# Performance work log

Measured on AMD Instinct MI355X. Metric: run time of the kernel, lower is better.

The kernel has to match this reference:

```python
import jax, jax.numpy as jnp
import numpy as np

H = 512      # hidden == embed (required: process-block LSTM consumes attention output of size hidden)
XY = 2
CITY_T = 100
BATCH = 512
INIT = 0.08  # uniform(-0.08, 0.08) weight init


def _unif(key, shape):
    return jax.random.uniform(key, shape, jnp.float32, minval=-INIT, maxval=INIT)


def lstm_cell(x, h, c, Wih, Whh, bih, bhh):
    # PyTorch gate order: i, f, g, o
    g = x @ Wih.T + h @ Whh.T + (bih + bhh)
    i, f, gg, o = jnp.split(g, 4, axis=-1)
    c_new = jax.nn.sigmoid(f) * c + jax.nn.sigmoid(i) * jnp.tanh(gg)
    h_new = jax.nn.sigmoid(o) * jnp.tanh(c_new)
    return h_new, c_new


def setup_inputs() -> dict:
    key = jax.random.key(0)
    ks = jax.random.split(key, 20)
    inp = {
        "x": jax.random.uniform(ks[0], (BATCH, CITY_T, XY), jnp.float32),      # city coords in [0,1)
        "dec_i1": jax.random.uniform(ks[1], (BATCH, H), jnp.float32),          # torch.rand(batch,1,hidden)
        "W_emb": _unif(ks[2], (H, XY)),
        "enc_Wih": _unif(ks[3], (4 * H, H)),
        "enc_Whh": _unif(ks[4], (4 * H, H)),
        "enc_bih": _unif(ks[5], (4 * H,)),
        "enc_bhh": _unif(ks[6], (4 * H,)),
        "dec_Wih": _unif(ks[7], (4 * H, H)),
        "dec_Whh": _unif(ks[8], (4 * H, H)),
        "dec_bih": _unif(ks[9], (4 * H,)),
        "dec_bhh": _unif(ks[10], (4 * H,)),
        "W_q": _unif(ks[11], (H, H)),
        "W_ref": _unif(ks[12], (H, H)),
        "v": _unif(ks[13], (1, H)),       # Vec: Linear(hidden,1,bias=False)
        "fc1": _unif(ks[14], (H, H)),
        "fc2": _unif(ks[15], (1, H)),
    }
    return inp


def reference(x, dec_i1, W_emb, enc_Wih, enc_Whh, enc_bih, enc_bhh,
              dec_Wih, dec_Whh, dec_bih, dec_bhh, W_q, W_ref, v, fc1, fc2):
    batch, city_t, _ = x.shape
    emb = x @ W_emb.T                                   # (b, c, H)

    # ---- Encoder LSTM (zero initial state) ----
    h0 = jnp.zeros((batch, H), emb.dtype)
    c0 = jnp.zeros((batch, H), emb.dtype)

    def enc_step(carry, xt):
        h, c = carry
        h, c = lstm_cell(xt, h, c, enc_Wih, enc_Whh, enc_bih, enc_bhh)
        return (h, c), h

    (hT, cT), enc_h = jax.lax.scan(enc_step, (h0, c0), jnp.swapaxes(emb, 0, 1))
    enc_h = jnp.swapaxes(enc_h, 0, 1)                   # (b, c, H)

    # W_ref(enc_h) is static across decode steps -> compute once
    u1 = enc_h @ W_ref.T                                # (b, c, H)

    # ---- Decoder: city_t steps of LSTM cell + Bahdanau attention ----
    def dec_step(carry, _):
        dec_i, h, c = carry
        h, c = lstm_cell(dec_i, h, c, dec_Wih, dec_Whh, dec_bih, dec_bhh)
        u2 = h @ W_q.T                                  # (b, H)
        u = jnp.tanh(u1 + u2[:, None, :]) @ v[0]        # (b, c)
        a = jax.nn.softmax(u, axis=1)
        d = jnp.einsum('bc,bch->bh', a, enc_h)          # glimpse (b, H)
        return (d, h, c), None

    (_, h_last, _), _ = jax.lax.scan(dec_step, (dec_i1, hT, cT), None, length=city_t)

    # final2FC: Linear->ReLU->Linear -> scalar per batch
    pred_l = jax.nn.relu(h_last @ fc1.T) @ fc2.T        # (b, 1)
    return pred_l[:, 0]
```

## Files before the change

kernel.cpp:

```cpp
#include <hip/hip_runtime.h>
#include <hip/hip_bf16.h>

#define H 512
#define TSTEPS 100
#define BATCH 512
#define KB 16
#define NBLK 256
#define NT 1024
#define NGRP 8
#define GBLK 32

typedef __attribute__((ext_vector_type(8))) short bf16x8;
typedef __attribute__((ext_vector_type(8))) unsigned short u16x8;
typedef __attribute__((ext_vector_type(4))) float f32x4;
typedef unsigned short u16;

__device__ __forceinline__ float bf2f(u16 u) {
    union { unsigned int i; float f; } z; z.i = ((unsigned int)u) << 16; return z.f;
}
__device__ __forceinline__ u16 f2bf(float f) {
    union { float f; unsigned int u; } z; z.f = f;
    unsigned int r = (z.u + 0x7fffu + ((z.u >> 16) & 1u)) >> 16;
    return (u16)r;
}
__device__ __forceinline__ float sigmoidf_(float x) { return 1.0f / (1.0f + __expf(-x)); }
__device__ __forceinline__ float ftanh(float x) {
    x = fminf(15.0f, fmaxf(-15.0f, x));
    float e = __expf(2.0f * x);
    return (e - 1.0f) / (e + 1.0f);
}
__device__ __forceinline__ f32x4 MF(bf16x8 a, bf16x8 b, f32x4 c) {
    return __builtin_amdgcn_mfma_f32_16x16x32_bf16(a, b, c, 0, 0, 0);
}

__device__ __forceinline__ size_t pidx(int m, int k) {
    int kb = k >> 5, kin = k & 31;
    int lane = (m & 15) + (((kin >> 2) & 3) << 4);
    int j = (kin & 3) + ((kin >> 4) << 2);
    return ((size_t)((m >> 4) * KB + kb) * 64 + lane) * 8 + j;
}

__device__ __forceinline__ void gbar32(unsigned* bar, int grp) {
    __syncthreads();
    if (threadIdx.x == 0) {
        unsigned* cnt = &bar[grp * 32];
        unsigned* gen = &bar[grp * 32 + 16];
        unsigned g = __hip_atomic_load(gen, __ATOMIC_RELAXED, __HIP_MEMORY_SCOPE_AGENT);
        if (__hip_atomic_fetch_add(cnt, 1u, __ATOMIC_ACQ_REL, __HIP_MEMORY_SCOPE_AGENT) == GBLK - 1u) {
            __hip_atomic_store(cnt, 0u, __ATOMIC_RELAXED, __HIP_MEMORY_SCOPE_AGENT);
            __hip_atomic_fetch_add(gen, 1u, __ATOMIC_ACQ_REL, __HIP_MEMORY_SCOPE_AGENT);
        } else {
            while (__hip_atomic_load(gen, __ATOMIC_RELAXED, __HIP_MEMORY_SCOPE_AGENT) == g) {
                __builtin_amdgcn_s_sleep(2);
            }
            __threadfence();
        }
    }
    __syncthreads();
}

__global__ void prep_kernel(const float* __restrict__ W_emb, const float* __restrict__ enc_Wih,
                            const float* __restrict__ enc_bih, const float* __restrict__ enc_bhh,
                            const float* __restrict__ dec_bih, const float* __restrict__ dec_bhh,
                            float* __restrict__ Wc, float* __restrict__ bc, float* __restrict__ db) {
    int g = blockIdx.x * blockDim.x + threadIdx.x;
    if (g >= 4 * H) return;
    float s0 = 0.f, s1 = 0.f;
    for (int j = 0; j < H; ++j) {
        float w = enc_Wih[(size_t)g * H + j];
        s0 += w * W_emb[j * 2 + 0];
        s1 += w * W_emb[j * 2 + 1];
    }
    Wc[g * 2 + 0] = s0; Wc[g * 2 + 1] = s1;
    bc[g] = enc_bih[g] + enc_bhh[g];
    db[g] = dec_bih[g] + dec_bhh[g];
}

__global__ void pack_w(const float* __restrict__ W, u16* __restrict__ hi, u16* __restrict__ lo,
                       int total) {
    int idx = blockIdx.x * 256 + threadIdx.x;
    if (idx >= total) return;
    int m = idx >> 9, k = idx & 511;
    float v = W[idx];
    u16 h16 = f2bf(v);
    u16 l16 = f2bf(v - bf2f(h16));
    size_t p = pidx(m, k);
    hi[p] = h16; lo[p] = l16;
}

__global__ void zero4(float* __restrict__ p, int n) {
    int i = blockIdx.x * blockDim.x + threadIdx.x;
    if (i < n) p[i] = 0.f;
}

__global__ __launch_bounds__(NT, 1) void persist_enc(
    const float* __restrict__ x, const float* __restrict__ Wc, const float* __restrict__ bc,
    const u16* __restrict__ WeH, const u16* __restrict__ WeL,
    float* __restrict__ cbuf, u16* __restrict__ hbuf,
    u16* __restrict__ ench, unsigned* __restrict__ bar) {
    extern __shared__ char smem[];
    u16* wlds = (u16*)smem;
    float* exch = (float*)(smem + 131072);
    const int tid = threadIdx.x;
    const int lane = tid & 63;
    const int w = tid >> 6;
    const int q = w & 3, j = w >> 2;
    const int blk = blockIdx.x;
    const int grp = blk & 7, nni = blk >> 3;
    const size_t BHs = (size_t)BATCH * H;

    for (int c = 0; c < 8; ++c) {
        int cq = c >> 1, hl = c & 1;
        const u16x8* s8 = (const u16x8*)((hl ? WeL : WeH) + (size_t)((cq * 32 + nni) * KB) * 512);
        u16x8* d8 = (u16x8*)(wlds + c * 8192);
        for (int i = tid; i < 1024; i += NT) d8[i] = s8[i];
    }
    __syncthreads();

    for (int t = 0; t < TSTEPS; ++t) {
        const u16* Ah = hbuf + (size_t)(t & 1) * 2 * BHs;
        const u16* Al = Ah + BHs;
        u16* Hh = hbuf + (size_t)((t + 1) & 1) * 2 * BHs;
        u16* Hl = Hh + BHs;
        f32x4 acc = {};
#pragma unroll 4
        for (int kb = 0; kb < KB; ++kb) {
            bf16x8 bh = *(const bf16x8*)&wlds[((q * 2 + 0) * KB + kb) * 512 + lane * 8];
            bf16x8 bl = *(const bf16x8*)&wlds[((q * 2 + 1) * KB + kb) * 512 + lane * 8];
            size_t ab = ((size_t)((grp * 4 + j) * KB + kb) * 64 + lane) * 8;
            bf16x8 ah = *(const bf16x8*)&Ah[ab];
            bf16x8 al = *(const bf16x8*)&Al[ab];
            acc = MF(ah, bh, acc);
            acc = MF(ah, bl, acc);
            acc = MF(al, bh, acc);
        }
        const int col = lane & 15, rg = lane >> 4;
#pragma unroll
        for (int r = 0; r < 4; ++r)
            exch[(q * 64 + j * 16 + rg * 4 + r) * 16 + col] = acc[r];
        __syncthreads();
        {
            int lb = tid >> 4, cl = tid & 15;
            int b = grp * 64 + lb, n = nni * 16 + cl;
            float x0 = x[((size_t)b * TSTEPS + t) * 2 + 0];
            float x1 = x[((size_t)b * TSTEPS + t) * 2 + 1];
            float g[4];
#pragma unroll
            for (int qq = 0; qq < 4; ++qq)
                g[qq] = exch[(qq * 64 + lb) * 16 + cl] + bc[qq * H + n]
                      + x0 * Wc[(qq * H + n) * 2 + 0] + x1 * Wc[(qq * H + n) * 2 + 1];
            size_t ci = (size_t)b * H + n;
            float cn = sigmoidf_(g[1]) * cbuf[ci] + sigmoidf_(g[0]) * ftanh(g[2]);
            float hn = sigmoidf_(g[3]) * ftanh(cn);
            cbuf[ci] = cn;
            u16 hh = f2bf(hn), hl16 = f2bf(hn - bf2f(hh));
            size_t p = pidx(b, n);
            Hh[p] = hh; Hl[p] = hl16;
            ench[((size_t)b * TSTEPS + t) * H + n] = hh;
        }
        gbar32(bar, grp);
    }
}

__global__ __launch_bounds__(NT, 1) void persist_dec(
    const u16* __restrict__ WdiH, const u16* __restrict__ WdiL,
    const u16* __restrict__ WdhH, const u16* __restrict__ WdhL,
    const float* __restrict__ db,
    const u16* __restrict__ WqH, const u16* __restrict__ WqL,
    const u16* __restrict__ u1r, const u16* __restrict__ ench, const float* __restrict__ vv,
    float* __restrict__ cbuf, u16* __restrict__ hbuf,
    u16* __restrict__ dhi, u16* __restrict__ dlo,
    unsigned* __restrict__ bar) {
    extern __shared__ char smem[];
    u16* wlds = (u16*)smem;
    char* scratch = smem + 131072;
    float* exch  = (float*)scratch;
    float* u2row = (float*)scratch;
    float* ssc   = (float*)(scratch + 4096);
    float* ssm   = (float*)(scratch + 4928);
    f32x4* dacc  = (f32x4*)(scratch + 5760);
    const int tid = threadIdx.x;
    const int lane = tid & 63;
    const int w = tid >> 6;
    const int blk = blockIdx.x;
    const int grp = blk & 7, nni = blk >> 3;
    const size_t BHs = (size_t)BATCH * H;

    float vvr[8];
    {
        float4 v0 = *(const float4*)&vv[lane * 8];
        float4 v1 = *(const float4*)&vv[lane * 8 + 4];
        vvr[0] = v0.x; vvr[1] = v0.y; vvr[2] = v0.z; vvr[3] = v0.w;
        vvr[4] = v1.x; vvr[5] = v1.y; vvr[6] = v1.z; vvr[7] = v1.w;
    }

    for (int c = 0; c < 8; ++c) {
        int mat = c >> 2, cq = c & 3;
        const u16x8* s8 = (const u16x8*)((mat ? WdhH : WdiH) + (size_t)((cq * 32 + nni) * KB) * 512);
        u16x8* d8 = (u16x8*)(wlds + c * 8192);
        for (int i = tid; i < 1024; i += NT) d8[i] = s8[i];
    }
    __syncthreads();

    for (int s = 0; s < TSTEPS; ++s) {
        {
            const u16* hAh = hbuf + (size_t)(s & 1) * 2 * BHs;
            const u16* hAl = hAh + BHs;
            u16* Hh = hbuf + (size_t)((s + 1) & 1) * 2 * BHs;
            u16* Hl = Hh + BHs;
            const int q = w & 3, j = w >> 2;
            f32x4 acc = {};
#pragma unroll
            for (int ph = 0; ph < 2; ++ph) {
                const u16* Ah = ph ? hAh : dhi;
                const u16* Al = ph ? hAl : dlo;
                const u16* Wl = ph ? WdhL : WdiL;
#pragma unroll 4
                for (int kb = 0; kb < KB; ++kb) {
                    bf16x8 bh = *(const bf16x8*)&wlds[((ph * 4 + q) * KB + kb) * 512 + lane * 8];
                    bf16x8 bl = *(const bf16x8*)&Wl[((size_t)((q * 32 + nni) * KB + kb) * 64 + lane) * 8];
                    size_t ab = ((size_t)((grp * 4 + j) * KB + kb) * 64 + lane) * 8;
                    bf16x8 ah = *(const bf16x8*)&Ah[ab];
                    bf16x8 al = *(const bf16x8*)&Al[ab];
                    acc = MF(ah, bh, acc);
                    acc = MF(ah, bl, acc);
                    acc = MF(al, bh, acc);
                }
            }
            const int col = lane & 15, rg = lane >> 4;
#pragma unroll
            for (int r = 0; r < 4; ++r)
                exch[(q * 64 + j * 16 + rg * 4 + r) * 16 + col] = acc[r];
            __syncthreads();
            {
                int lb = tid >> 4, cl = tid & 15;
                int b = grp * 64 + lb, n = nni * 16 + cl;
                float g[4];
#pragma unroll
                for (int qq = 0; qq < 4; ++qq)
                    g[qq] = exch[(qq * 64 + lb) * 16 + cl] + db[qq * H + n];
                size_t ci = (size_t)b * H + n;
                float cn = sigmoidf_(g[1]) * cbuf[ci] + sigmoidf_(g[0]) * ftanh(g[2]);
                float hn = sigmoidf_(g[3]) * ftanh(cn);
                cbuf[ci] = cn;
                u16 hh = f2bf(hn), hl16 = f2bf(hn - bf2f(hh));
                size_t p = pidx(b, n);
                Hh[p] = hh; Hl[p] = hl16;
            }
        }
        if (s == TSTEPS - 1) break;
        gbar32(bar, grp);

        {
            const u16* Ah = hbuf + (size_t)((s + 1) & 1) * 2 * BHs;
            const u16* Al = Ah + BHs;
            const int mf = grp * 4 + (nni >> 3);
            f32x4 acc[2] = {};
#pragma unroll 4
            for (int kb = 0; kb < KB; ++kb) {
                size_t ab = ((size_t)(mf * KB + kb) * 64 + lane) * 8;
                bf16x8 ah = *(const bf16x8*)&Ah[ab];
                bf16x8 al = *(const bf16x8*)&Al[ab];
#pragma unroll
                for (int f = 0; f < 2; ++f) {
                    int n16 = w * 2 + f;
                    size_t fb = ((size_t)(n16 * KB + kb) * 64 + lane) * 8;
                    bf16x8 bh = *(const bf16x8*)&WqH[fb];
                    bf16x8 bl = *(const bf16x8*)&WqL[fb];
                    acc[f] = MF(ah, bh, acc[f]);
                    acc[f] = MF(ah, bl, acc[f]);
                    acc[f] = MF(al, bh, acc[f]);
                }
            }
            const int col = lane & 15, rg = lane >> 4;
            const int t0 = (nni & 7) * 2;
#pragma unroll
            for (int f = 0; f < 2; ++f)
#pragma unroll
                for (int r = 0; r < 4; ++r) {
                    int m = rg * 4 + r;
                    int n = (w * 2 + f) * 16 + col;
                    if (m == t0)     u2row[n] = acc[f][r];
                    if (m == t0 + 1) u2row[512 + n] = acc[f][r];
                }
        }
        __syncthreads();
        {
            const int r = tid >> 9;
            const int par = (tid >> 6) & 7;
            const int cnt = (par < 4) ? 13 : 12;
            const int b = grp * 64 + 2 * nni + r;
            float u2v[8];
            {
                float4 a0 = *(const float4*)&u2row[r * 512 + lane * 8];
                float4 a1 = *(const float4*)&u2row[r * 512 + lane * 8 + 4];
                u2v[0] = a0.x; u2v[1] = a0.y; u2v[2] = a0.z; u2v[3] = a0.w;
                u2v[4] = a1.x; u2v[5] = a1.y; u2v[6] = a1.z; u2v[7] = a1.w;
            }
            const u16* u1base = &u1r[(size_t)b * TSTEPS * H + lane * 8];
            const u16* ehbase = &ench[(size_t)b * TSTEPS * H + lane * 8];
            for (int i0 = 0; i0 < 13; i0 += 5) {
                u16x8 uvv[5];
#pragma unroll
                for (int u = 0; u < 5; ++u) {
                    int i = i0 + u;
                    if (i < cnt)
                        uvv[u] = *(const u16x8*)&u1base[(size_t)(par + 8 * i) * H];
                }
#pragma unroll
                for (int u = 0; u < 5; ++u) {
                    int i = i0 + u;
                    if (i < cnt) {
                        float pp = 0.f;
#pragma unroll
                        for (int jj = 0; jj < 8; ++jj)
                            pp += vvr[jj] * ftanh(bf2f(uvv[u][jj]) + u2v[jj]);
#pragma unroll
                        for (int off = 32; off; off >>= 1) pp += __shfl_xor(pp, off);
                        if (lane == 0) ssc[r * 100 + par + 8 * i] = pp;
                    }
                }
            }
            __syncthreads();
            if (tid < 128) {
                int r2 = tid >> 6, ln = tid & 63;
                float s1 = ssc[r2 * 100 + ln];
                float s2 = (ln + 64 < 100) ? ssc[r2 * 100 + ln + 64] : -1e30f;
                float m = fmaxf(s1, s2);
#pragma unroll
                for (int off = 32; off; off >>= 1) m = fmaxf(m, __shfl_xor(m, off));
                float e1 = __expf(s1 - m);
                float e2 = (ln + 64 < 100) ? __expf(s2 - m) : 0.f;
                float sum = e1 + e2;
#pragma unroll
                for (int off = 32; off; off >>= 1) sum += __shfl_xor(sum, off);
                float inv = 1.f / sum;
                ssm[r2 * 100 + ln] = e1 * inv;
                if (ln + 64 < 100) ssm[r2 * 100 + ln + 64] = e2 * inv;
            }
            __syncthreads();
            float ga[8] = {};
            for (int i0 = 0; i0 < 13; i0 += 5) {
                u16x8 evv[5];
#pragma unroll
                for (int u = 0; u < 5; ++u) {
                    int i = i0 + u;
                    if (i < cnt)
                        evv[u] = *(const u16x8*)&ehbase[(size_t)(par + 8 * i) * H];
                }
#pragma unroll
                for (int u = 0; u < 5; ++u) {
                    int i = i0 + u;
                    if (i < cnt) {
                        float a = ssm[r * 100 + par + 8 * i];
#pragma unroll
                        for (int jj = 0; jj < 8; ++jj) ga[jj] += a * bf2f(evv[u][jj]);
                    }
                }
            }
            f32x4 g0 = {ga[0], ga[1], ga[2], ga[3]};
            f32x4 g1 = {ga[4], ga[5], ga[6], ga[7]};
            if (par < 4) {
                dacc[(((par * 2 + r) * 64) + lane) * 2 + 0] = g0;
                dacc[(((par * 2 + r) * 64) + lane) * 2 + 1] = g1;
            }
            __syncthreads();
            if (par >= 4) {
                int slot = par - 4;
                f32x4 t0 = dacc[(((slot * 2 + r) * 64) + lane) * 2 + 0];
                f32x4 t1 = dacc[(((slot * 2 + r) * 64) + lane) * 2 + 1];
                dacc[(((slot * 2 + r) * 64) + lane) * 2 + 0] = t0 + g0;
                dacc[(((slot * 2 + r) * 64) + lane) * 2 + 1] = t1 + g1;
            }
            __syncthreads();
            if (tid < 128) {
                int r2 = tid >> 6, l = tid & 63;
                float fin[8];
#pragma unroll
                for (int jj = 0; jj < 8; ++jj) fin[jj] = 0.f;
#pragma unroll
                for (int sl = 0; sl < 4; ++sl) {
                    f32x4 d0 = dacc[(((sl * 2 + r2) * 64) + l) * 2 + 0];
                    f32x4 d1 = dacc[(((sl * 2 + r2) * 64) + l) * 2 + 1];
                    fin[0] += d0[0]; fin[1] += d0[1]; fin[2] += d0[2]; fin[3] += d0[3];
                    fin[4] += d1[0]; fin[5] += d1[1]; fin[6] += d1[2]; fin[7] += d1[3];
                }
                int b2 = grp * 64 + 2 * nni + r2;
                int h0 = l * 8;
#pragma unroll
                for (int qd = 0; qd < 2; ++qd) {
                    int k = h0 + 4 * qd;
                    size_t p = (((size_t)(b2 >> 4) * KB + (k >> 5)) * 64 + (b2 & 15)
                                + (((k >> 2) & 3) << 4)) * 8 + (((k >> 4) & 1) << 2);
                    float f0 = fin[4 * qd], f1 = fin[4 * qd + 1], f2 = fin[4 * qd + 2], f3 = fin[4 * qd + 3];
                    u16 a0 = f2bf(f0), a1 = f2bf(f1), a2 = f2bf(f2), a3 = f2bf(f3);
                    *(ushort4*)&dhi[p] = make_ushort4(a0, a1, a2, a3);
                    u16 c0 = f2bf(f0 - bf2f(a0)), c1 = f2bf(f1 - bf2f(a1));
                    u16 c2 = f2bf(f2 - bf2f(a2)), c3 = f2bf(f3 - bf2f(a3));
                    *(ushort4*)&dlo[p] = make_ushort4(c0, c1, c2, c3);
                }
            }
        }
        gbar32(bar, grp);
    }
}

__global__ __launch_bounds__(256) void gemm_u1(const u16* __restrict__ ench_row,
                                               const u16* __restrict__ Bh, const u16* __restrict__ Bl,
                                               u16* __restrict__ u1_row) {
    __shared__ u16 lds[2 * KB * 64 * 8];
    const int tid = threadIdx.x;
    const int m0 = blockIdx.x * 32;
    {
        int r = tid >> 3;
        int o = tid & 7;
#pragma unroll
        for (int p8 = 0; p8 < 8; ++p8) {
            int k0 = (o + 8 * p8) * 8;
            const u16* src = &ench_row[(size_t)(m0 + r) * H + k0];
            ushort4 v0 = *(const ushort4*)&src[0];
            ushort4 v1 = *(const ushort4*)&src[4];
            int kb = k0 >> 5, kin0 = k0 & 31;
            int g0 = (kin0 >> 2) & 3;
            int jo = (kin0 >> 4) << 2;
            u16* base = &lds[(size_t)(((r >> 4) * KB + kb) * 64) * 8];
            *(ushort4*)&base[((r & 15) + 16 * g0) * 8 + jo] = v0;
            *(ushort4*)&base[((r & 15) + 16 * (g0 + 1)) * 8 + jo] = v1;
        }
    }
    __syncthreads();
    const int lane = tid & 63;
    const int w = tid >> 6;
    const int mw = w & 1, nh = w >> 1;
    for (int nc = 0; nc < 16; ++nc) {
        int n16 = nh * 16 + nc;
        f32x4 acc = {};
#pragma unroll 4
        for (int kb = 0; kb < KB; ++kb) {
            bf16x8 a = *(const bf16x8*)&lds[((mw * KB + kb) * 64 + lane) * 8];
            size_t fb = ((size_t)(n16 * KB + kb) * 64 + lane) * 8;
            bf16x8 bh = *(const bf16x8*)&Bh[fb];
            bf16x8 bl = *(const bf16x8*)&Bl[fb];
            acc = MF(a, bh, acc);
            acc = MF(a, bl, acc);
        }
        const int col = lane & 15, rg = lane >> 4;
#pragma unroll
        for (int r = 0; r < 4; ++r) {
            size_t mrow = (size_t)m0 + mw * 16 + rg * 4 + r;
            u1_row[mrow * H + n16 * 16 + col] = f2bf(acc[r]);
        }
    }
}

__global__ __launch_bounds__(256) void final_kernel(const u16* __restrict__ hi,
                                                    const u16* __restrict__ lo,
                                                    const float* __restrict__ fc1,
                                                    const float* __restrict__ fc2,
                                                    float* __restrict__ out) {
    const int b = blockIdx.x;
    __shared__ float hsh[H];
    __shared__ float red[256];
    for (int i = threadIdx.x; i < H; i += 256) {
        size_t p = pidx(b, i);
        hsh[i] = bf2f(hi[p]) + bf2f(lo[p]);
    }
    __syncthreads();
    float total = 0.f;
    for (int n = threadIdx.x; n < H; n += 256) {
        float acc = 0.f;
        for (int j = 0; j < H; ++j) acc += fc1[(size_t)n * H + j] * hsh[j];
        total += fmaxf(acc, 0.f) * fc2[n];
    }
    red[threadIdx.x] = total;
    __syncthreads();
    for (int s = 128; s > 0; s >>= 1) {
        if (threadIdx.x < s) red[threadIdx.x] += red[threadIdx.x + s];
        __syncthreads();
    }
    if (threadIdx.x == 0) out[b] = red[0];
}

extern "C" void kernel_launch(void* const* d_in, const int* in_sizes, int n_in,
                              void* d_out, int out_size, void* d_ws, size_t ws_size,
                              hipStream_t stream) {
    (void)in_sizes; (void)n_in; (void)out_size;
    const float* x       = (const float*)d_in[0];
    const float* dec_i1  = (const float*)d_in[1];
    const float* W_emb   = (const float*)d_in[2];
    const float* enc_Wih = (const float*)d_in[3];
    const float* enc_Whh = (const float*)d_in[4];
    const float* enc_bih = (const float*)d_in[5];
    const float* enc_bhh = (const float*)d_in[6];
    const float* dec_Wih = (const float*)d_in[7];
    const float* dec_Whh = (const float*)d_in[8];
    const float* dec_bih = (const float*)d_in[9];
    const float* dec_bhh = (const float*)d_in[10];
    const float* W_q     = (const float*)d_in[11];
    const float* W_ref   = (const float*)d_in[12];
    const float* vv      = (const float*)d_in[13];
    const float* fc1     = (const float*)d_in[14];
    const float* fc2     = (const float*)d_in[15];
    float* out = (float*)d_out;

    const size_t BH = (size_t)BATCH * H;
    const size_t W4 = (size_t)4 * H * H;
    const size_t WS = (size_t)H * H;
    const size_t TBH = (size_t)TSTEPS * BATCH * H;

    unsigned* bar = (unsigned*)d_ws;
    float* c_  = (float*)d_ws + 256;
    u16* hbuf  = (u16*)(c_ + BH);
    float* Wc  = (float*)(hbuf + 4 * BH);
    float* bc  = Wc + 4 * H * 2;
    float* db  = bc + 4 * H;
    u16* dhi   = (u16*)(db + 4 * H);
    u16* dlo   = dhi + BH;
    u16* WeH   = dlo + BH;    u16* WeL  = WeH + W4;
    u16* WdiH  = WeL + W4;    u16* WdiL = WdiH + W4;
    u16* WdhH  = WdiL + W4;   u16* WdhL = WdhH + W4;
    u16* WqH   = WdhL + W4;   u16* WqL  = WqH + WS;
    u16* WrH   = WqL + WS;    u16* WrL  = WrH + WS;
    u16* ench  = WrL + WS;
    u16* u1r   = ench + TBH;

    size_t needed = (size_t)((char*)(u1r + TBH) - (char*)d_ws);
    if (ws_size < needed) return;

    const int ENC_SMEM = 131072 + 16384;
    const int DEC_SMEM = 131072 + 22528;
    (void)hipFuncSetAttribute((const void*)persist_enc, hipFuncAttributeMaxDynamicSharedMemorySize, ENC_SMEM);
    (void)hipFuncSetAttribute((const void*)persist_dec, hipFuncAttributeMaxDynamicSharedMemorySize, DEC_SMEM);

    prep_kernel<<<8, 256, 0, stream>>>(W_emb, enc_Wih, enc_bih, enc_bhh, dec_bih, dec_bhh, Wc, bc, db);
    pack_w<<<(int)(W4 / 256), 256, 0, stream>>>(enc_Whh, WeH, WeL, (int)W4);
    pack_w<<<(int)(W4 / 256), 256, 0, stream>>>(dec_Wih, WdiH, WdiL, (int)W4);
    pack_w<<<(int)(W4 / 256), 256, 0, stream>>>(dec_Whh, WdhH, WdhL, (int)W4);
    pack_w<<<(int)(WS / 256), 256, 0, stream>>>(W_q, WqH, WqL, (int)WS);
    pack_w<<<(int)(WS / 256), 256, 0, stream>>>(W_ref, WrH, WrL, (int)WS);
    pack_w<<<(int)(BH / 256), 256, 0, stream>>>(dec_i1, dhi, dlo, (int)BH);
    zero4<<<(int)((256 + 3 * BH + 255) / 256), 256, 0, stream>>>((float*)d_ws, (int)(256 + 3 * BH));

    persist_enc<<<NBLK, NT, ENC_SMEM, stream>>>(x, Wc, bc, WeH, WeL, c_, hbuf, ench, bar);
    gemm_u1<<<TSTEPS * BATCH / 32, 256, 0, stream>>>(ench, WrH, WrL, u1r);
    persist_dec<<<NBLK, NT, DEC_SMEM, stream>>>(WdiH, WdiL, WdhH, WdhL, db, WqH, WqL,
                                                u1r, ench, vv, c_, hbuf, dhi, dlo, bar);
    final_kernel<<<BATCH, 256, 0, stream>>>(hbuf, hbuf + BH, fc1, fc2, out);
}
```

Baseline: 12.25 ms.

## Replace counter grid barrier with per-block flag barrier and prefetch glimpse rows

Replaces the atomic counter/generation group barrier with a flag-array barrier: each block publishes a monotonically increasing step value and one wavefront polls all 32 flags in its group at once. This removes contention on a single counter and the serial last-arriver release. The decoder also issues the first eight enc_h row loads before the u2 GEMM, so their latency overlaps the MFMA work. In exchange it uses more registers, and the flag regions need separate buffers and a larger zeroed workspace.

```diff
diff --git a/kernel.cpp b/kernel.cpp
--- a/kernel.cpp
+++ b/kernel.cpp
@@ -40,21 +40,23 @@
     return ((size_t)((m >> 4) * KB + kb) * 64 + lane) * 8 + j;
 }
 
-__device__ __forceinline__ void gbar32(unsigned* bar, int grp) {
-    __syncthreads();
-    if (threadIdx.x == 0) {
-        unsigned* cnt = &bar[grp * 32];
-        unsigned* gen = &bar[grp * 32 + 16];
-        unsigned g = __hip_atomic_load(gen, __ATOMIC_RELAXED, __HIP_MEMORY_SCOPE_AGENT);
-        if (__hip_atomic_fetch_add(cnt, 1u, __ATOMIC_ACQ_REL, __HIP_MEMORY_SCOPE_AGENT) == GBLK - 1u) {
-            __hip_atomic_store(cnt, 0u, __ATOMIC_RELAXED, __HIP_MEMORY_SCOPE_AGENT);
-            __hip_atomic_fetch_add(gen, 1u, __ATOMIC_ACQ_REL, __HIP_MEMORY_SCOPE_AGENT);
-        } else {
-            while (__hip_atomic_load(gen, __ATOMIC_RELAXED, __HIP_MEMORY_SCOPE_AGENT) == g) {
-                __builtin_amdgcn_s_sleep(2);
-            }
-            __threadfence();
-        }
+__device__ __forceinline__ void fbar(unsigned* flags, int grp, int bib, unsigned target) {
+    __syncthreads();
+    if (threadIdx.x < 64) {
+        if (threadIdx.x == 0)
+            __hip_atomic_store(&flags[(grp * 32 + bib) * 16], target,
+                               __ATOMIC_RELEASE, __HIP_MEMORY_SCOPE_AGENT);
+        const int l = threadIdx.x;
+        bool done;
+        do {
+            unsigned v = target;
+            if (l < 32)
+                v = __hip_atomic_load(&flags[(grp * 32 + l) * 16],
+                                      __ATOMIC_RELAXED, __HIP_MEMORY_SCOPE_AGENT);
+            done = __all((int)(v >= target));
+            if (!done) __builtin_amdgcn_s_sleep(1);
+        } while (!done);
+        __threadfence();
     }
     __syncthreads();
 }
@@ -97,7 +99,7 @@
     const float* __restrict__ x, const float* __restrict__ Wc, const float* __restrict__ bc,
     const u16* __restrict__ WeH, const u16* __restrict__ WeL,
     float* __restrict__ cbuf, u16* __restrict__ hbuf,
-    u16* __restrict__ ench, unsigned* __restrict__ bar) {
+    u16* __restrict__ ench, unsigned* __restrict__ fE) {
     extern __shared__ char smem[];
     u16* wlds = (u16*)smem;
     float* exch = (float*)(smem + 131072);
@@ -158,7 +160,7 @@
             Hh[p] = hh; Hl[p] = hl16;
             ench[((size_t)b * TSTEPS + t) * H + n] = hh;
         }
-        gbar32(bar, grp);
+        fbar(fE, grp, nni, (unsigned)(t + 1));
     }
 }
 
@@ -170,7 +172,7 @@
     const u16* __restrict__ u1r, const u16* __restrict__ ench, const float* __restrict__ vv,
     float* __restrict__ cbuf, u16* __restrict__ hbuf,
     u16* __restrict__ dhi, u16* __restrict__ dlo,
-    unsigned* __restrict__ bar) {
+    unsigned* __restrict__ fA, unsigned* __restrict__ fC) {
     extern __shared__ char smem[];
     u16* wlds = (u16*)smem;
     char* scratch = smem + 131072;
@@ -249,47 +251,55 @@
             }
         }
         if (s == TSTEPS - 1) break;
-        gbar32(bar, grp);
-
-        {
-            const u16* Ah = hbuf + (size_t)((s + 1) & 1) * 2 * BHs;
-            const u16* Al = Ah + BHs;
-            const int mf = grp * 4 + (nni >> 3);
-            f32x4 acc[2] = {};
-#pragma unroll 4
-            for (int kb = 0; kb < KB; ++kb) {
-                size_t ab = ((size_t)(mf * KB + kb) * 64 + lane) * 8;
-                bf16x8 ah = *(const bf16x8*)&Ah[ab];
-                bf16x8 al = *(const bf16x8*)&Al[ab];
-#pragma unroll
-                for (int f = 0; f < 2; ++f) {
-                    int n16 = w * 2 + f;
-                    size_t fb = ((size_t)(n16 * KB + kb) * 64 + lane) * 8;
-                    bf16x8 bh = *(const bf16x8*)&WqH[fb];
-                    bf16x8 bl = *(const bf16x8*)&WqL[fb];
-                    acc[f] = MF(ah, bh, acc[f]);
-                    acc[f] = MF(ah, bl, acc[f]);
-                    acc[f] = MF(al, bh, acc[f]);
-                }
-            }
-            const int col = lane & 15, rg = lane >> 4;
-            const int t0 = (nni & 7) * 2;
-#pragma unroll
-            for (int f = 0; f < 2; ++f)
-#pragma unroll
-                for (int r = 0; r < 4; ++r) {
-                    int m = rg * 4 + r;
-                    int n = (w * 2 + f) * 16 + col;
-                    if (m == t0)     u2row[n] = acc[f][r];
-                    if (m == t0 + 1) u2row[512 + n] = acc[f][r];
-                }
-        }
-        __syncthreads();
+        fbar(fA, grp, nni, (unsigned)(s + 1));
+
         {
             const int r = tid >> 9;
             const int par = (tid >> 6) & 7;
             const int cnt = (par < 4) ? 13 : 12;
-            const int b = grp * 64 + 2 * nni + r;
+            const int brow = grp * 64 + 2 * nni + r;
+            const u16* u1base = &u1r[(size_t)brow * TSTEPS * H + lane * 8];
+            const u16* ehbase = &ench[(size_t)brow * TSTEPS * H + lane * 8];
+            u16x8 evA[8];
+#pragma unroll
+            for (int u = 0; u < 8; ++u)
+                evA[u] = *(const u16x8*)&ehbase[(size_t)(par + 8 * u) * H];
+
+            {
+                const u16* Ah = hbuf + (size_t)((s + 1) & 1) * 2 * BHs;
+                const u16* Al = Ah + BHs;
+                const int mf = grp * 4 + (nni >> 3);
+                f32x4 acc[2] = {};
+#pragma unroll 4
+                for (int kb = 0; kb < KB; ++kb) {
+                    size_t ab = ((size_t)(mf * KB + kb) * 64 + lane) * 8;
+                    bf16x8 ah = *(const bf16x8*)&Ah[ab];
+                    bf16x8 al = *(const bf16x8*)&Al[ab];
+#pragma unroll
+                    for (int f = 0; f < 2; ++f) {
+                        int n16 = w * 2 + f;
+                        size_t fb = ((size_t)(n16 * KB + kb) * 64 + lane) * 8;
+                        bf16x8 bh = *(const bf16x8*)&WqH[fb];
+                        bf16x8 bl = *(const bf16x8*)&WqL[fb];
+                        acc[f] = MF(ah, bh, acc[f]);
+                        acc[f] = MF(ah, bl, acc[f]);
+                        acc[f] = MF(al, bh, acc[f]);
+                    }
+                }
+                const int col = lane & 15, rg = lane >> 4;
+                const int t0 = (nni & 7) * 2;
+#pragma unroll
+                for (int f = 0; f < 2; ++f)
+#pragma unroll
+                    for (int rr = 0; rr < 4; ++rr) {
+                        int m = rg * 4 + rr;
+                        int n = (w * 2 + f) * 16 + col;
+                        if (m == t0)     u2row[n] = acc[f][rr];
+                        if (m == t0 + 1) u2row[512 + n] = acc[f][rr];
+                    }
+            }
+            __syncthreads();
+
             float u2v[8];
             {
                 float4 a0 = *(const float4*)&u2row[r * 512 + lane * 8];
@@ -297,8 +307,6 @@
                 u2v[0] = a0.x; u2v[1] = a0.y; u2v[2] = a0.z; u2v[3] = a0.w;
                 u2v[4] = a1.x; u2v[5] = a1.y; u2v[6] = a1.z; u2v[7] = a1.w;
             }
-            const u16* u1base = &u1r[(size_t)b * TSTEPS * H + lane * 8];
-            const u16* ehbase = &ench[(size_t)b * TSTEPS * H + lane * 8];
             for (int i0 = 0; i0 < 13; i0 += 5) {
                 u16x8 uvv[5];
 #pragma unroll
@@ -340,21 +348,27 @@
             }
             __syncthreads();
             float ga[8] = {};
-            for (int i0 = 0; i0 < 13; i0 += 5) {
-                u16x8 evv[5];
+#pragma unroll
+            for (int u = 0; u < 8; ++u) {
+                float a = ssm[r * 100 + par + 8 * u];
+#pragma unroll
+                for (int jj = 0; jj < 8; ++jj) ga[jj] += a * bf2f(evA[u][jj]);
+            }
+            {
+                u16x8 evB[5];
 #pragma unroll
                 for (int u = 0; u < 5; ++u) {
-                    int i = i0 + u;
+                    int i = 8 + u;
                     if (i < cnt)
-                        evv[u] = *(const u16x8*)&ehbase[(size_t)(par + 8 * i) * H];
+                        evB[u] = *(const u16x8*)&ehbase[(size_t)(par + 8 * i) * H];
                 }
 #pragma unroll
                 for (int u = 0; u < 5; ++u) {
-                    int i = i0 + u;
+                    int i = 8 + u;
                     if (i < cnt) {
                         float a = ssm[r * 100 + par + 8 * i];
 #pragma unroll
-                        for (int jj = 0; jj < 8; ++jj) ga[jj] += a * bf2f(evv[u][jj]);
+                        for (int jj = 0; jj < 8; ++jj) ga[jj] += a * bf2f(evB[u][jj]);
                     }
                 }
             }
@@ -401,7 +415,7 @@
                 }
             }
         }
-        gbar32(bar, grp);
+        fbar(fC, grp, nni, (unsigned)(s + 1));
     }
 }
 
@@ -508,8 +522,10 @@
     const size_t WS = (size_t)H * H;
     const size_t TBH = (size_t)TSTEPS * BATCH * H;
 
-    unsigned* bar = (unsigned*)d_ws;
-    float* c_  = (float*)d_ws + 256;
+    unsigned* fA = (unsigned*)d_ws;
+    unsigned* fC = fA + 4096;
+    unsigned* fE = fC + 4096;
+    float* c_  = (float*)(fE + 4096);
     u16* hbuf  = (u16*)(c_ + BH);
     float* Wc  = (float*)(hbuf + 4 * BH);
     float* bc  = Wc + 4 * H * 2;
@@ -539,11 +555,11 @@
     pack_w<<<(int)(WS / 256), 256, 0, stream>>>(W_q, WqH, WqL, (int)WS);
     pack_w<<<(int)(WS / 256), 256, 0, stream>>>(W_ref, WrH, WrL, (int)WS);
     pack_w<<<(int)(BH / 256), 256, 0, stream>>>(dec_i1, dhi, dlo, (int)BH);
-    zero4<<<(int)((256 + 3 * BH + 255) / 256), 256, 0, stream>>>((float*)d_ws, (int)(256 + 3 * BH));
-
-    persist_enc<<<NBLK, NT, ENC_SMEM, stream>>>(x, Wc, bc, WeH, WeL, c_, hbuf, ench, bar);
+    zero4<<<(int)((12288 + 3 * BH + 255) / 256), 256, 0, stream>>>((float*)d_ws, (int)(12288 + 3 * BH));
+
+    persist_enc<<<NBLK, NT, ENC_SMEM, stream>>>(x, Wc, bc, WeH, WeL, c_, hbuf, ench, fE);
     gemm_u1<<<TSTEPS * BATCH / 32, 256, 0, stream>>>(ench, WrH, WrL, u1r);
     persist_dec<<<NBLK, NT, DEC_SMEM, stream>>>(WdiH, WdiL, WdhH, WdhL, db, WqH, WqL,
-                                                u1r, ench, vv, c_, hbuf, dhi, dlo, bar);
+                                                u1r, ench, vv, c_, hbuf, dhi, dlo, fA, fC);
     final_kernel<<<BATCH, 256, 0, stream>>>(hbuf, hbuf + BH, fc1, fc2, out);
 }
```

New measurement: 11.27 ms (median of 2 runs). -8.0%, faster.
